# Kernel tuning notes

Hardware: AMD Instinct MI355X
Metric: run time of the kernel (lower is better)

The kernel has to match this reference:

```python
import math
import jax, jax.numpy as jnp
import numpy as np

B, L, C, H = 32, 320, 768, 12
LENS_T = 64
KEEP_RATIO = 0.7
AD_H = 64   # Mixer adapter bottleneck width (assumed bottleneck adapter)
EPS = 1e-5  # torch LayerNorm default


def _ln(x, g, b):
    m = jnp.mean(x, axis=-1, keepdims=True)
    v = jnp.mean((x - m) ** 2, axis=-1, keepdims=True)
    return (x - m) * jax.lax.rsqrt(v + EPS) * g + b


def _attention(x, qkv_w, proj_w, proj_b):
    b, l, c = x.shape
    dh = c // H
    qkv = (x @ qkv_w).reshape(b, l, 3, H, dh)
    q = jnp.transpose(qkv[:, :, 0], (0, 2, 1, 3))  # [B,H,L,Dh]
    k = jnp.transpose(qkv[:, :, 1], (0, 2, 1, 3))
    v = jnp.transpose(qkv[:, :, 2], (0, 2, 1, 3))
    a = jax.nn.softmax(jnp.einsum('bhid,bhjd->bhij', q * (dh ** -0.5), k), axis=-1)
    out = jnp.einsum('bhij,bhjd->bhid', a, v).transpose(0, 2, 1, 3).reshape(b, l, c)
    return out @ proj_w + proj_b, a


def _mixer(x, dw, db, uw, ub):
    return jax.nn.gelu(x @ dw + db, approximate=False) @ uw + ub


def _mlp(x, w1, b1, w2, b2):
    return jax.nn.gelu(x @ w1 + b1, approximate=False) @ w2 + b2


def _ce(attn, tokens, lens_t, lens_keep, gidx):
    # attn: [B,H,Lt+Ls,Lt+Ls]; average template->search block over heads and template rows
    attn_t = jnp.mean(attn[:, :, :lens_t, lens_t:], axis=(1, 2))  # [B, Ls]
    order = jnp.argsort(-attn_t, axis=1)                          # descending sort indices
    topk_idx, rest_idx = order[:, :lens_keep], order[:, lens_keep:]
    keep = jnp.take_along_axis(gidx, topk_idx, axis=1)
    removed = jnp.take_along_axis(gidx, rest_idx, axis=1)
    kept_tok = jnp.take_along_axis(tokens[:, lens_t:], topk_idx[..., None], axis=1)
    return jnp.concatenate([tokens[:, :lens_t], kept_tok], axis=1), keep, removed


def setup_inputs():
    key = jax.random.key(0)
    ks = jax.random.split(key, 12)
    p = lambda k, shape: jax.random.normal(k, shape, jnp.float32) * 0.02
    ls = L - LENS_T
    return {
        'x': jax.random.normal(ks[0], (B, L, C), jnp.float32),
        'xi': jax.random.normal(ks[1], (B, L, C), jnp.float32),
        'gi_t': jnp.arange(B * LENS_T, dtype=jnp.int32).reshape(B, LENS_T),
        'gi_ti': jnp.arange(B * LENS_T, dtype=jnp.int32).reshape(B, LENS_T),
        'gi_s': jnp.arange(B * ls, dtype=jnp.int32).reshape(B, ls),
        'gi_si': jnp.arange(B * ls, dtype=jnp.int32).reshape(B, ls),
        'layer': 0,
        'n1_g': jnp.ones((C,), jnp.float32), 'n1_b': jnp.zeros((C,), jnp.float32),
        'qkv_w': p(ks[2], (C, 3 * C)),
        'proj_w': p(ks[3], (C, C)), 'proj_b': jnp.zeros((C,), jnp.float32),
        'n2_g': jnp.ones((C,), jnp.float32), 'n2_b': jnp.zeros((C,), jnp.float32),
        'fc1_w': p(ks[4], (C, 4 * C)), 'fc1_b': jnp.zeros((4 * C,), jnp.float32),
        'fc2_w': p(ks[5], (4 * C, C)), 'fc2_b': jnp.zeros((C,), jnp.float32),
        'ad1_dw': p(ks[6], (C, AD_H)), 'ad1_db': jnp.zeros((AD_H,), jnp.float32),
        'ad1_uw': p(ks[7], (AD_H, C)), 'ad1_ub': jnp.zeros((C,), jnp.float32),
        'ad2_dw': p(ks[8], (C, AD_H)), 'ad2_db': jnp.zeros((AD_H,), jnp.float32),
        'ad2_uw': p(ks[9], (AD_H, C)), 'ad2_ub': jnp.zeros((C,), jnp.float32),
    }


def reference(x, xi, gi_t, gi_ti, gi_s, gi_si, layer,
              n1_g, n1_b, qkv_w, proj_w, proj_b, n2_g, n2_b,
              fc1_w, fc1_b, fc2_w, fc2_b,
              ad1_dw, ad1_db, ad1_uw, ad1_ub, ad2_dw, ad2_db, ad2_uw, ad2_ub):
    # layer not in {3,6,9}: Mixer-adapter path, then candidate elimination, then MLP
    xori = x
    xa, attn = _attention(_ln(x, n1_g, n1_b), qkv_w, proj_w, proj_b)
    x = x + xa + _mixer(_ln(xi, n1_g, n1_b), ad1_dw, ad1_db, ad1_uw, ad1_ub)
    xia, i_attn = _attention(_ln(xi, n1_g, n1_b), qkv_w, proj_w, proj_b)
    xi = xi + xia + _mixer(_ln(xori, n1_g, n1_b), ad1_dw, ad1_db, ad1_uw, ad1_ub)
    lens_t = gi_t.shape[1]
    lens_s = x.shape[1] - lens_t
    lens_keep = math.ceil(KEEP_RATIO * lens_s)  # 180
    x, gi_s, removed = _ce(attn, x, lens_t, lens_keep, gi_s)
    xi, gi_si, removedi = _ce(i_attn, xi, lens_t, lens_keep, gi_si)
    xori = x
    x = x + _mlp(_ln(x, n2_g, n2_b), fc1_w, fc1_b, fc2_w, fc2_b) \
          + _mixer(_ln(xi, n2_g, n2_b), ad2_dw, ad2_db, ad2_uw, ad2_ub)
    xi = xi + _mlp(_ln(xi, n2_g, n2_b), fc1_w, fc1_b, fc2_w, fc2_b) \
            + _mixer(_ln(xori, n2_g, n2_b), ad2_dw, ad2_db, ad2_uw, ad2_ub)
    return (x, gi_t, gi_s, removed, attn, xi, gi_ti, gi_si, removedi, i_attn)
```

## Files before the change

### kernel.cpp

```cpp
#include <hip/hip_runtime.h>
#include <hip/hip_bf16.h>

#define NB   32
#define LL   320
#define CC   768
#define NH   12
#define DHD  64
#define LT   64
#define LSN  256
#define NKEEP 180
#define NREM  76
#define LP   244
#define ADH  64
#define C4   3072

typedef __attribute__((ext_vector_type(8))) short s16x8;
typedef __attribute__((ext_vector_type(4))) float f32x4;

__device__ __forceinline__ ushort f2b(float f){
  union { __hip_bfloat16 h; ushort u; } cv;
  cv.h = __float2bfloat16(f);
  return cv.u;
}

__device__ __forceinline__ void glds16(const ushort* g, ushort* l){
  __builtin_amdgcn_global_load_lds(
      (const __attribute__((address_space(1))) void*)g,
      (__attribute__((address_space(3))) void*)l, 16, 0, 0);
}

__device__ __forceinline__ float blk_sum(float v, float* sh){
  #pragma unroll
  for (int o = 32; o > 0; o >>= 1) v += __shfl_down(v, o, 64);
  int w = threadIdx.x >> 6;
  if ((threadIdx.x & 63) == 0) sh[w] = v;
  __syncthreads();
  float r = sh[0] + sh[1] + sh[2] + sh[3];
  __syncthreads();
  return r;
}

__global__ __launch_bounds__(256) void ln_k(const float* __restrict__ x,
                                            const float* __restrict__ g,
                                            const float* __restrict__ be,
                                            float* __restrict__ y,
                                            ushort* __restrict__ yb,
                                            float* __restrict__ lnt){
  __shared__ float sh[4];
  size_t row = blockIdx.x;
  const float* xr = x + row * CC;
  int t = threadIdx.x;
  float v0 = xr[t], v1 = xr[t + 256], v2 = xr[t + 512];
  float m = blk_sum(v0 + v1 + v2, sh) * (1.0f / 768.0f);
  float d0 = v0 - m, d1 = v1 - m, d2 = v2 - m;
  float var = blk_sum(d0*d0 + d1*d1 + d2*d2, sh) * (1.0f / 768.0f);
  float rs = rsqrtf(var + 1e-5f);
  float o0 = d0 * rs * g[t]       + be[t];
  float o1 = d1 * rs * g[t + 256] + be[t + 256];
  float o2 = d2 * rs * g[t + 512] + be[t + 512];
  float* yr = y + row * CC;
  yr[t] = o0; yr[t + 256] = o1; yr[t + 512] = o2;
  if (yb){
    ushort* yr2 = yb + row * CC;
    yr2[t] = f2b(o0); yr2[t + 256] = f2b(o1); yr2[t + 512] = f2b(o2);
  }
  if (lnt){
    int i = (int)(row % LL);
    if (i < 64){
      float* lr = lnt + ((row / LL) * 64 + i) * CC;
      lr[t] = o0; lr[t + 256] = o1; lr[t + 512] = o2;
    }
  }
}

__global__ __launch_bounds__(256) void gemm2_k(
    const float* __restrict__ A1, const float* __restrict__ W1,
    float* __restrict__ C1, ushort* __restrict__ Cb1,
    const float* __restrict__ A2, const float* __restrict__ W2,
    float* __restrict__ C2,
    int K, int ldw, int ldc, int ysplit)
{
  __shared__ float As[32*128];
  __shared__ float Bs[32*128];
  const int t = threadIdx.x;
  const int tx = t & 15, ty = t >> 4;
  const int n0 = blockIdx.x * 128;
  const int yb = blockIdx.y;
  const float* A; const float* W; float* Cm; ushort* Cb; int m0;
  if (yb < ysplit){ A = A1; W = W1; Cm = C1; Cb = Cb1; m0 = yb * 128; }
  else            { A = A2; W = W2; Cm = C2; Cb = nullptr; m0 = (yb - ysplit) * 128; }

  float acc[8][8] = {};
  for (int k0 = 0; k0 < K; k0 += 32){
    #pragma unroll
    for (int q = 0; q < 4; q++){
      int idx = t + q*256;
      int m = idx & 127, kq = idx >> 7;
      float4 v = *reinterpret_cast<const float4*>(A + (size_t)(m0+m)*K + k0 + kq*4);
      As[(kq*4+0)*128 + m] = v.x; As[(kq*4+1)*128 + m] = v.y;
      As[(kq*4+2)*128 + m] = v.z; As[(kq*4+3)*128 + m] = v.w;
    }
    #pragma unroll
    for (int q = 0; q < 4; q++){
      int idx = t + q*256;
      int kr = idx >> 5, nq = idx & 31;
      float4 v = *reinterpret_cast<const float4*>(W + (size_t)(k0+kr)*ldw + n0 + nq*4);
      *reinterpret_cast<float4*>(&Bs[kr*128 + nq*4]) = v;
    }
    __syncthreads();
    #pragma unroll
    for (int kk = 0; kk < 32; kk++){
      float a[8], b[8];
      *reinterpret_cast<float4*>(&a[0]) = *reinterpret_cast<float4*>(&As[kk*128 + ty*4]);
      *reinterpret_cast<float4*>(&a[4]) = *reinterpret_cast<float4*>(&As[kk*128 + 64 + ty*4]);
      *reinterpret_cast<float4*>(&b[0]) = *reinterpret_cast<float4*>(&Bs[kk*128 + tx*4]);
      *reinterpret_cast<float4*>(&b[4]) = *reinterpret_cast<float4*>(&Bs[kk*128 + 64 + tx*4]);
      #pragma unroll
      for (int i = 0; i < 8; i++)
        #pragma unroll
        for (int j = 0; j < 8; j++)
          acc[i][j] = fmaf(a[i], b[j], acc[i][j]);
    }
    __syncthreads();
  }
  #pragma unroll
  for (int i = 0; i < 8; i++){
    int m = m0 + ty*4 + (i & 3) + (i >> 2) * 64;
    #pragma unroll
    for (int j = 0; j < 8; j++){
      int n = n0 + tx*4 + (j & 3) + (j >> 2) * 64;
      float v = acc[i][j];
      Cm[(size_t)m * ldc + n] = v;
      if (Cb) Cb[(size_t)m * ldc + n] = f2b(v);
    }
  }
}

template<bool GELU, bool ACC, bool OBF>
__global__ __launch_bounds__(256) void mg_k(
    const ushort* __restrict__ A, const ushort* __restrict__ Wt,
    const float* __restrict__ bias, void* __restrict__ Cp,
    int M, int N, int K,
    const float* __restrict__ res0, const float* __restrict__ res1, int Mhalf,
    const ushort* __restrict__ A2_0, const ushort* __restrict__ A2_1,
    const ushort* __restrict__ W2t, int K2, const float* __restrict__ bias2,
    void* __restrict__ Cp1)
{
  __shared__ __align__(16) ushort Asm[128*32];
  __shared__ __align__(16) ushort Bsm[128*32];
  const int t = threadIdx.x;
  const int m0 = blockIdx.y * 128, n0 = blockIdx.x * 128;
  const int wave = t >> 6, lane = t & 63;
  const int wrow = wave >> 1, wcol = wave & 1;
  const int lr = lane & 15, ks = lane >> 4;
  const int srow = lane >> 2, scp = lane & 3;

  f32x4 acc[4][4];
  #pragma unroll
  for (int i = 0; i < 4; i++)
    #pragma unroll
    for (int j = 0; j < 4; j++)
      #pragma unroll
      for (int r = 0; r < 4; r++) acc[i][j][r] = 0.f;

  const int nseg = W2t ? 2 : 1;
  for (int seg = 0; seg < nseg; seg++){
    const ushort* Abase; const ushort* Bbase; int ldA, ldB, Ks;
    if (seg == 0){
      Abase = A + (size_t)m0 * K; ldA = K; Bbase = Wt; ldB = K; Ks = K;
    } else {
      Abase = (res1 && m0 >= Mhalf) ? (A2_1 + (size_t)(m0 - Mhalf) * K2)
                                    : (A2_0 + (size_t)m0 * K2);
      ldA = K2; Bbase = W2t; ldB = K2; Ks = K2;
    }
    for (int k0 = 0; k0 < Ks; k0 += 32){
      #pragma unroll
      for (int q = 0; q < 2; q++){
        int r16 = wave*32 + q*16;
        int row = r16 + srow;
        int sch = scp ^ ((row >> 1) & 3);
        glds16(Abase + (size_t)row * ldA + k0 + sch*8, &Asm[r16*32]);
        int rbn = n0 + row; if (rbn > N-1) rbn = N-1;
        glds16(Bbase + (size_t)rbn * ldB + k0 + sch*8, &Bsm[r16*32]);
      }
      __syncthreads();
      s16x8 af[4], bf[4];
      #pragma unroll
      for (int f = 0; f < 4; f++){
        int ra = wrow*64 + f*16 + lr;
        af[f] = *reinterpret_cast<const s16x8*>(&Asm[ra*32 + ((ks ^ ((ra>>1)&3))<<3)]);
        int rbn = wcol*64 + f*16 + lr;
        bf[f] = *reinterpret_cast<const s16x8*>(&Bsm[rbn*32 + ((ks ^ ((rbn>>1)&3))<<3)]);
      }
      #pragma unroll
      for (int i = 0; i < 4; i++)
        #pragma unroll
        for (int j = 0; j < 4; j++)
          acc[i][j] = __builtin_amdgcn_mfma_f32_16x16x32_bf16(af[i], bf[j], acc[i][j], 0, 0, 0);
      __syncthreads();
    }
  }
  #pragma unroll
  for (int i = 0; i < 4; i++){
    int mb = m0 + wrow*64 + i*16 + ks*4;
    #pragma unroll
    for (int j = 0; j < 4; j++){
      int n = n0 + wcol*64 + j*16 + lr;
      if (n >= N) continue;
      float bv = (bias ? bias[n] : 0.0f) + (bias2 ? bias2[n] : 0.0f);
      #pragma unroll
      for (int r = 0; r < 4; r++){
        int mrow = mb + r;
        float v = acc[i][j][r] + bv;
        if (GELU) v = 0.5f * v * (1.0f + erff(v * 0.70710678118654752f));
        if (res0){
          if (res1 && mrow >= Mhalf) v += res1[(size_t)(mrow - Mhalf) * N + n];
          else                       v += res0[(size_t)mrow * N + n];
        }
        if (Cp1 && mrow >= Mhalf){
          size_t idx = (size_t)(mrow - Mhalf) * N + n;
          if (OBF)      ((ushort*)Cp1)[idx] = f2b(v);
          else if (ACC) ((float*)Cp1)[idx] += v;
          else          ((float*)Cp1)[idx]  = v;
        } else {
          size_t idx = (size_t)mrow * N + n;
          if (OBF)      ((ushort*)Cp)[idx] = f2b(v);
          else if (ACC) ((float*)Cp)[idx] += v;
          else          ((float*)Cp)[idx]  = v;
        }
      }
    }
  }
}

__global__ __launch_bounds__(256) void tconv_k(const float* __restrict__ W,
                                               ushort* __restrict__ Wt,
                                               int K, int N, int ldw, int colOff){
  __shared__ float tile[32][33];
  int t = threadIdx.x;
  int tx = t & 31, ty = t >> 5;
  int k0 = blockIdx.y * 32, n0 = blockIdx.x * 32;
  #pragma unroll
  for (int q = 0; q < 4; q++)
    tile[ty + 8*q][tx] = W[(size_t)(k0 + ty + 8*q) * ldw + colOff + n0 + tx];
  __syncthreads();
  #pragma unroll
  for (int q = 0; q < 4; q++)
    Wt[(size_t)(n0 + ty + 8*q) * K + k0 + tx] = f2b(tile[tx][ty + 8*q]);
}

__global__ __launch_bounds__(256) void scorest_k(const float* __restrict__ qt,
                                                 const float* __restrict__ kf,
                                                 float* __restrict__ p0,
                                                 float* __restrict__ p1){
  __shared__ float Qs[16][65];
  __shared__ float Ks[16][65];
  const int t = threadIdx.x, tx = t & 15, ty = t >> 4;
  const int s = blockIdx.y;
  const int bh = blockIdx.z; const int b = bh / NH, h = bh % NH;
  const int j0 = blockIdx.x * 64;
  float* sc = s ? p1 : p0;
  const float* qts = qt + (size_t)s * NB * 64 * CC;
  const float* kfs = kf + (size_t)s * NB * LL * CC;
  const size_t qbase = (size_t)b * 64 * CC + (size_t)h * 64;
  const size_t kbase = (size_t)b * LL * CC + (size_t)h * 64;
  const int lkk = t & 15, lmm = t >> 4;
  float acc[4][4] = {};
  for (int d0 = 0; d0 < DHD; d0 += 16){
    #pragma unroll
    for (int q = 0; q < 4; q++)
      Qs[lkk][lmm + 16*q] = qts[qbase + (size_t)(lmm + 16*q) * CC + d0 + lkk];
    #pragma unroll
    for (int q = 0; q < 4; q++)
      Ks[lkk][lmm + 16*q] = kfs[kbase + (size_t)(j0 + lmm + 16*q) * CC + d0 + lkk];
    __syncthreads();
    #pragma unroll
    for (int kk = 0; kk < 16; kk++){
      float a[4], b2[4];
      #pragma unroll
      for (int i = 0; i < 4; i++) a[i] = Qs[kk][ty*4 + i];
      #pragma unroll
      for (int j = 0; j < 4; j++) b2[j] = Ks[kk][tx*4 + j];
      #pragma unroll
      for (int i = 0; i < 4; i++)
        #pragma unroll
        for (int j = 0; j < 4; j++)
          acc[i][j] = fmaf(a[i], b2[j], acc[i][j]);
    }
    __syncthreads();
  }
  #pragma unroll
  for (int i = 0; i < 4; i++)
    #pragma unroll
    for (int j = 0; j < 4; j++)
      sc[((size_t)bh * LL + ty*4 + i) * LL + j0 + tx*4 + j] = acc[i][j] * 0.125f;
}

__global__ __launch_bounds__(256) void sqs_k(const ushort* __restrict__ qv,
                                             const ushort* __restrict__ kb,
                                             float* __restrict__ p0,
                                             float* __restrict__ p1){
  __shared__ ushort Qs[64][72];
  __shared__ ushort Ks[64][72];
  const int t = threadIdx.x;
  const int it = blockIdx.x, bh = blockIdx.y, s = blockIdx.z;
  const int b = bh / NH, h = bh % NH;
  const int w = t >> 6, lane = t & 63;
  const int lr = lane & 15, ks = lane >> 4;
  float* sc = s ? p1 : p0;
  const int qrow0 = s * NB * LL + b * LL + 64 + it * 64;
  const int krow0 = s * NB * LL + b * LL;

  #pragma unroll
  for (int q = 0; q < 4; q++){
    int idx = t + q*256;
    int row = idx >> 4, dv = idx & 15;
    *reinterpret_cast<ushort4*>(&Qs[row][dv*4]) =
      *reinterpret_cast<const ushort4*>(qv + (size_t)(qrow0 + row) * 1536 + h*64 + dv*4);
  }

  f32x4 acc[5][4];
  #pragma unroll
  for (int jt = 0; jt < 5; jt++)
    #pragma unroll
    for (int n = 0; n < 4; n++)
      #pragma unroll
      for (int r = 0; r < 4; r++) acc[jt][n][r] = 0.f;

  for (int jt = 0; jt < 5; jt++){
    __syncthreads();
    #pragma unroll
    for (int q = 0; q < 4; q++){
      int idx = t + q*256;
      int row = idx >> 4, dv = idx & 15;
      *reinterpret_cast<ushort4*>(&Ks[row][dv*4]) =
        *reinterpret_cast<const ushort4*>(kb + (size_t)(krow0 + jt*64 + row) * CC + h*64 + dv*4);
    }
    __syncthreads();
    #pragma unroll
    for (int n = 0; n < 4; n++)
      #pragma unroll
      for (int kt = 0; kt < 2; kt++){
        s16x8 a  = *reinterpret_cast<const s16x8*>(&Qs[w*16 + lr][kt*32 + ks*8]);
        s16x8 bb = *reinterpret_cast<const s16x8*>(&Ks[n*16 + lr][kt*32 + ks*8]);
        acc[jt][n] = __builtin_amdgcn_mfma_f32_16x16x32_bf16(a, bb, acc[jt][n], 0, 0, 0);
      }
  }
  #pragma unroll
  for (int jt = 0; jt < 5; jt++)
    #pragma unroll
    for (int n = 0; n < 4; n++)
      #pragma unroll
      for (int r = 0; r < 4; r++) acc[jt][n][r] *= 0.125f;
  #pragma unroll
  for (int r = 0; r < 4; r++){
    float mx = -3.4e38f;
    #pragma unroll
    for (int jt = 0; jt < 5; jt++)
      #pragma unroll
      for (int n = 0; n < 4; n++) mx = fmaxf(mx, acc[jt][n][r]);
    #pragma unroll
    for (int o = 1; o < 16; o <<= 1) mx = fmaxf(mx, __shfl_xor(mx, o, 64));
    float sum = 0.f;
    #pragma unroll
    for (int jt = 0; jt < 5; jt++)
      #pragma unroll
      for (int n = 0; n < 4; n++){
        float e = expf(acc[jt][n][r] - mx);
        acc[jt][n][r] = e; sum += e;
      }
    #pragma unroll
    for (int o = 1; o < 16; o <<= 1) sum += __shfl_xor(sum, o, 64);
    float inv = 1.0f / sum;
    size_t rowbase = ((size_t)bh * LL + 64 + it*64 + w*16 + ks*4 + r) * LL;
    #pragma unroll
    for (int jt = 0; jt < 5; jt++)
      #pragma unroll
      for (int n = 0; n < 4; n++)
        sc[rowbase + jt*64 + n*16 + lr] = acc[jt][n][r] * inv;
  }
}

__global__ __launch_bounds__(256) void softmaxt_k(float* __restrict__ p0,
                                                  float* __restrict__ p1){
  const int lane = threadIdx.x & 63;
  const int s = blockIdx.x / (NB*NH*16);
  const int bx = blockIdx.x % (NB*NH*16);
  const int bh = bx >> 4;
  const int i0 = (bx & 15) * 4;
  float* sc = s ? p1 : p0;
  const size_t row = (size_t)bh * LL + i0 + (threadIdx.x >> 6);
  float* sr = sc + row * LL;
  float v[5]; float mx = -3.4e38f;
  #pragma unroll
  for (int i = 0; i < 5; i++){ v[i] = sr[lane + 64*i]; mx = fmaxf(mx, v[i]); }
  #pragma unroll
  for (int o = 32; o > 0; o >>= 1) mx = fmaxf(mx, __shfl_xor(mx, o, 64));
  float s2 = 0.f;
  #pragma unroll
  for (int i = 0; i < 5; i++){ v[i] = expf(v[i] - mx); s2 += v[i]; }
  #pragma unroll
  for (int o = 32; o > 0; o >>= 1) s2 += __shfl_xor(s2, o, 64);
  float inv = 1.0f / s2;
  #pragma unroll
  for (int i = 0; i < 5; i++) sr[lane + 64*i] = v[i] * inv;
}

__global__ __launch_bounds__(256) void attnt1_k(const float* __restrict__ p0,
                                                const float* __restrict__ p1,
                                                double* __restrict__ pp){
  int g = blockIdx.x;
  int s = g / (NB*NH), bh = g % (NB*NH);
  int j = threadIdx.x;
  const float* probs = s ? p1 : p0;
  double sum = 0.0;
  for (int i = 0; i < LT; i++)
    sum += (double)probs[((size_t)bh * LL + i) * LL + 64 + j];
  pp[(size_t)g * LSN + j] = sum;
}
__global__ __launch_bounds__(256) void attnt2_k(const double* __restrict__ pp,
                                                float* __restrict__ at){
  int g = blockIdx.x;
  int j = threadIdx.x;
  double sum = 0.0;
  for (int h = 0; h < NH; h++)
    sum += pp[((size_t)g * NH + h) * LSN + j];
  at[g * LSN + j] = (float)(sum * (1.0 / 768.0));
}

__global__ __launch_bounds__(256) void pvm_k(const float* __restrict__ p0,
                                             const float* __restrict__ p1,
                                             const ushort* __restrict__ qv,
                                             ushort* __restrict__ pvb){
  __shared__ ushort Pa[64][72];
  __shared__ ushort Vt[64][72];
  const int t = threadIdx.x;
  const int bh = blockIdx.y, s = blockIdx.z;
  const int b = bh / NH, h = bh % NH;
  const int i0 = blockIdx.x * 64;
  const int w = t >> 6, lane = t & 63;
  const int lr = lane & 15, ks = lane >> 4;
  const float* Ap = (s ? p1 : p0) + (size_t)bh * LL * LL;
  const int vrow0 = s * NB * LL + b * LL;
  ushort* pvs = pvb + (size_t)s * NB * LL * CC;

  f32x4 acc[4];
  #pragma unroll
  for (int n = 0; n < 4; n++)
    #pragma unroll
    for (int r = 0; r < 4; r++) acc[n][r] = 0.f;

  for (int jt = 0; jt < 5; jt++){
    int j0 = jt * 64;
    #pragma unroll
    for (int q = 0; q < 4; q++){
      int idx = t + q*256;
      int i = idx >> 4, jv = idx & 15;
      float4 v = *reinterpret_cast<const float4*>(Ap + (size_t)(i0 + i) * LL + j0 + jv*4);
      ushort4 u; u.x = f2b(v.x); u.y = f2b(v.y); u.z = f2b(v.z); u.w = f2b(v.w);
      *reinterpret_cast<ushort4*>(&Pa[i][jv*4]) = u;
    }
    #pragma unroll
    for (int q = 0; q < 4; q++){
      int idx = t + q*256;
      int j = idx >> 4, dv = idx & 15;
      ushort4 u = *reinterpret_cast<const ushort4*>(
          qv + (size_t)(vrow0 + j0 + j) * 1536 + 768 + h*64 + dv*4);
      Vt[dv*4+0][j] = u.x; Vt[dv*4+1][j] = u.y;
      Vt[dv*4+2][j] = u.z; Vt[dv*4+3][j] = u.w;
    }
    __syncthreads();
    #pragma unroll
    for (int n = 0; n < 4; n++)
      #pragma unroll
      for (int kt = 0; kt < 2; kt++){
        s16x8 a = *reinterpret_cast<const s16x8*>(&Pa[w*16 + lr][kt*32 + ks*8]);
        s16x8 bb = *reinterpret_cast<const s16x8*>(&Vt[n*16 + lr][kt*32 + ks*8]);
        acc[n] = __builtin_amdgcn_mfma_f32_16x16x32_bf16(a, bb, acc[n], 0, 0, 0);
      }
    __syncthreads();
  }
  #pragma unroll
  for (int n = 0; n < 4; n++)
    #pragma unroll
    for (int r = 0; r < 4; r++){
      int i = w*16 + ks*4 + r;
      int d = n*16 + lr;
      pvs[(size_t)(b * LL + i0 + i) * 768 + h*64 + d] = f2b(acc[n][r]);
    }
}

__global__ __launch_bounds__(256) void init_ord_k(int* __restrict__ ordbuf, int n){
  int i = blockIdx.x * 256 + threadIdx.x;
  if (i < n) ordbuf[i] = i & 255;
}

__global__ __launch_bounds__(256) void ce_rank_k(const float* __restrict__ at,
                                                 int* __restrict__ ordbuf){
  __shared__ float a[256];
  int b = blockIdx.x, t = threadIdx.x;
  a[t] = at[b * LSN + t];
  __syncthreads();
  float mine = a[t];
  int rank = 0;
  for (int k = 0; k < 256; k++){
    float ak = a[k];
    rank += (ak > mine) || (ak == mine && k < t);
  }
  if (rank >= 0 && rank < 256) ordbuf[b * LSN + rank] = t;
}

__global__ __launch_bounds__(256) void ce_emit2_k(const int* __restrict__ ordbuf,
                                                  const int* __restrict__ g0,
                                                  const int* __restrict__ g1,
                                                  const int* __restrict__ t0,
                                                  const int* __restrict__ t1,
                                                  float* __restrict__ keep0,
                                                  float* __restrict__ keep1,
                                                  float* __restrict__ rem0,
                                                  float* __restrict__ rem1,
                                                  float* __restrict__ git0,
                                                  float* __restrict__ git1){
  int g = blockIdx.x, t = threadIdx.x;
  int s = g / NB, b = g % NB;
  const int* gidx = s ? g1 : g0;
  const int* gt   = s ? t1 : t0;
  float* out_keep = s ? keep1 : keep0;
  float* out_rem  = s ? rem1 : rem0;
  float* out_git  = s ? git1 : git0;
  int o = ordbuf[(size_t)g * LSN + t];
  o = min(max(o, 0), 255);
  int idx = gidx[b * LSN + o];
  if (t < NKEEP) out_keep[b * NKEEP + t] = (float)idx;
  else           out_rem[b * NREM + (t - NKEEP)] = (float)idx;
  if (t < LT)    out_git[b * LT + t] = (float)gt[b * LT + t];
}

__global__ __launch_bounds__(256) void gather_k(const float* __restrict__ xnew,
                                                const int* __restrict__ ordbuf,
                                                float* __restrict__ x2){
  int g = blockIdx.x;
  int s = g / (NB*LP), r0 = g % (NB*LP);
  int b = r0 / LP, r = r0 % LP;
  int o = (r < LT) ? 0 : ordbuf[(size_t)(s*NB + b) * LSN + (r - LT)];
  o = min(max(o, 0), 255);
  int src = (r < LT) ? r : (LT + o);
  const float* sp = xnew + (size_t)s * NB * LL * CC + ((size_t)b * LL + src) * CC;
  float* d = x2 + (size_t)s * NB * LP * CC + (size_t)r0 * CC;
  for (int i = threadIdx.x; i < CC; i += 256) d[i] = sp[i];
}

__global__ void sentinel_k(float* __restrict__ d, float val, int n){
  int i = blockIdx.x * 256 + threadIdx.x;
  if (i < n) d[i] = val;
}

extern "C" void kernel_launch(void* const* d_in, const int* in_sizes, int n_in,
                              void* d_out, int out_size, void* d_ws, size_t ws_size,
                              hipStream_t stream) {
  float* out = (float*)d_out;
  float* ws  = (float*)d_ws;

  static const int EXP[26] = {
    7864320, 7864320, 2048, 2048, 8192, 8192, 1,
    768, 768, 1769472, 589824, 768, 768, 768,
    2359296, 3072, 2359296, 768,
    49152, 64, 49152, 768, 49152, 64, 49152, 768 };

  const void* P[26];
  bool ok = false;
  if (n_in == 26){
    bool m = true; int bad = -1;
    for (int i = 0; i < 26; i++) if (in_sizes[i] != EXP[i]){ m = false; bad = i; break; }
    if (m){ for (int i = 0; i < 26; i++) P[i] = d_in[i]; ok = true; }
    else { sentinel_k<<<16, 256, 0, stream>>>(out, 20000.0f + 16.0f*bad, 4096); return; }
  } else if (n_in == 25){
    bool m = true; int bad = -1;
    for (int i = 0; i < 25; i++){
      int j = (i < 6) ? i : i + 1;
      if (in_sizes[i] != EXP[j]){ m = false; bad = i; break; }
    }
    if (m){
      for (int j = 0; j < 26; j++) P[j] = (j == 6) ? nullptr : d_in[(j < 6) ? j : j - 1];
      ok = true;
    } else { sentinel_k<<<16, 256, 0, stream>>>(out, 20000.0f + 16.0f*bad, 4096); return; }
  }
  if (!ok){ sentinel_k<<<16, 256, 0, stream>>>(out, 10000.0f + 8.0f*n_in, 4096); return; }
  if (out_size != 90656768){
    sentinel_k<<<16, 256, 0, stream>>>(out, 60000.0f + (float)(out_size / 1000000), 4096); return;
  }

  const float* x      = (const float*)P[0];
  const float* xi     = (const float*)P[1];
  const int*   gi_t   = (const int*)P[2];
  const int*   gi_ti  = (const int*)P[3];
  const int*   gi_s   = (const int*)P[4];
  const int*   gi_si  = (const int*)P[5];
  const float* n1_g   = (const float*)P[7];
  const float* n1_b   = (const float*)P[8];
  const float* qkv_w  = (const float*)P[9];
  const float* proj_w = (const float*)P[10];
  const float* proj_b = (const float*)P[11];
  const float* n2_g   = (const float*)P[12];
  const float* n2_b   = (const float*)P[13];
  const float* fc1_w  = (const float*)P[14];
  const float* fc1_b  = (const float*)P[15];
  const float* fc2_w  = (const float*)P[16];
  const float* fc2_b  = (const float*)P[17];
  const float* ad1_dw = (const float*)P[18];
  const float* ad1_db = (const float*)P[19];
  const float* ad1_uw = (const float*)P[20];
  const float* ad1_ub = (const float*)P[21];
  const float* ad2_dw = (const float*)P[22];
  const float* ad2_db = (const float*)P[23];
  const float* ad2_uw = (const float*)P[24];
  const float* ad2_ub = (const float*)P[25];

  const size_t o_x     = 0;
  const size_t o_git   = 5996544;
  const size_t o_gis   = 5998592;
  const size_t o_rem   = 6004352;
  const size_t o_attn  = 6006784;
  const size_t o_xi    = 45328384;
  const size_t o_giti  = 51324928;
  const size_t o_gisi  = 51326976;
  const size_t o_remi  = 51332736;
  const size_t o_iattn = 51335168;

  const size_t BLC      = (size_t)NB * LL * CC;
  const size_t BPC      = (size_t)NB * LP * CC;
  const size_t off_ln   = 0;
  const size_t off_l1b  = off_ln  + 2*BLC;
  const size_t off_k    = off_l1b + BLC;
  const size_t off_qv   = off_k   + 2*BLC;
  const size_t off_kb   = off_qv  + 2*BLC;
  const size_t off_lnt  = off_kb  + BLC;
  const size_t off_qt   = off_lnt + 3145728;
  const size_t off_xnew = off_qt  + 3145728;
  const size_t off_l2b  = off_xnew+ 2*BLC;
  const size_t off_mixh = off_l2b + BPC;
  const size_t off_att  = off_mixh+ 655360;
  const size_t off_attp = off_att + 16384;
  const size_t off_ord  = off_attp+ 393216;
  const size_t off_wts  = off_ord + 16384;
  const size_t total_f  = off_wts + 3342336;
  if (ws_size < total_f * sizeof(float)){
    sentinel_k<<<16, 256, 0, stream>>>(out, 40000.0f + (float)(ws_size >> 20), 4096);
    return;
  }

  int* ordbuf = (int*)(ws + off_ord);
  double* attp = (double*)(ws + off_attp);
  ushort* wts = (ushort*)(ws + off_wts);
  ushort* Wt_q    = wts;
  ushort* Wt_v    = wts + 589824;
  ushort* Wt_proj = wts + 1179648;
  ushort* Wt_fc1  = wts + 1769472;
  ushort* Wt_fc2  = wts + 4128768;
  ushort* Wt_a1d  = wts + 6488064;
  ushort* Wt_a1u  = wts + 6537216;
  ushort* Wt_a2d  = wts + 6586368;
  ushort* Wt_a2u  = wts + 6635520;
  ushort* ln1b = (ushort*)(ws + off_l1b);
  ushort* qvb  = (ushort*)(ws + off_qv);
  ushort* kb   = (ushort*)(ws + off_kb);
  ushort* pvb  = (ushort*)(ws + off_k);
  ushort* ln2b = (ushort*)(ws + off_l2b);
  ushort* mixhb= (ushort*)(ws + off_mixh);

  float* p0 = out + o_attn;
  float* p1 = out + o_iattn;

  tconv_k<<<dim3(24, 24), 256, 0, stream>>>(qkv_w,  Wt_q,    768, 768,  2304, 0);
  tconv_k<<<dim3(24, 24), 256, 0, stream>>>(qkv_w,  Wt_v,    768, 768,  2304, 1536);
  tconv_k<<<dim3(24, 24), 256, 0, stream>>>(proj_w, Wt_proj, 768, 768,  768,  0);
  tconv_k<<<dim3(96, 24), 256, 0, stream>>>(fc1_w,  Wt_fc1,  768, 3072, 3072, 0);
  tconv_k<<<dim3(24, 96), 256, 0, stream>>>(fc2_w,  Wt_fc2,  3072, 768, 768,  0);
  tconv_k<<<dim3(2,  24), 256, 0, stream>>>(ad1_dw, Wt_a1d,  768, 64,   64,   0);
  tconv_k<<<dim3(24, 2 ), 256, 0, stream>>>(ad1_uw, Wt_a1u,  64,  768,  768,  0);
  tconv_k<<<dim3(2,  24), 256, 0, stream>>>(ad2_dw, Wt_a2d,  768, 64,   64,   0);
  tconv_k<<<dim3(24, 2 ), 256, 0, stream>>>(ad2_uw, Wt_a2u,  64,  768,  768,  0);

  ln_k<<<NB*LL, 256, 0, stream>>>(x,  n1_g, n1_b, ws + off_ln, ln1b, ws + off_lnt);
  ln_k<<<NB*LL, 256, 0, stream>>>(xi, n1_g, n1_b, ws + off_ln + BLC,
                                  ln1b + (size_t)NB*LL*CC,
                                  ws + off_lnt + (size_t)NB*64*CC);
  mg_k<true,false,true><<<dim3(1, 160), 256, 0, stream>>>(
      ln1b, Wt_a1d, ad1_db, mixhb, 2*NB*LL, ADH, CC,
      nullptr, nullptr, 0, nullptr, nullptr, nullptr, 0, nullptr, nullptr);
  gemm2_k<<<dim3(6, 192), 256, 0, stream>>>(
      ws + off_ln, qkv_w + 768, ws + off_k, kb,
      ws + off_lnt, qkv_w, ws + off_qt,
      CC, 2304, CC, 160);
  mg_k<false,false,true><<<dim3(12, 160), 256, 0, stream>>>(
      ln1b, Wt_q, nullptr, qvb, 2*NB*LL, 1536, CC,
      nullptr, nullptr, 0, nullptr, nullptr, nullptr, 0, nullptr, nullptr);

  scorest_k<<<dim3(5, 2, NB*NH), 256, 0, stream>>>(ws + off_qt, ws + off_k, p0, p1);
  sqs_k<<<dim3(4, NB*NH, 2), 256, 0, stream>>>(qvb, kb, p0, p1);
  softmaxt_k<<<2*NB*NH*16, 256, 0, stream>>>(p0, p1);
  attnt1_k<<<2*NB*NH, 256, 0, stream>>>(p0, p1, attp);
  attnt2_k<<<2*NB, 256, 0, stream>>>(attp, ws + off_att);

  pvm_k<<<dim3(5, NB*NH, 2), 256, 0, stream>>>(p0, p1, qvb, pvb);
  mg_k<false,false,false><<<dim3(6, 160), 256, 0, stream>>>(
      pvb, Wt_proj, proj_b, ws + off_xnew, 2*NB*LL, CC, CC,
      x, xi, NB*LL,
      mixhb + (size_t)NB*LL*ADH, mixhb, Wt_a1u, ADH, ad1_ub, nullptr);

  init_ord_k<<<(2*NB*LSN + 255)/256, 256, 0, stream>>>(ordbuf, 2*NB*LSN);
  ce_rank_k<<<2*NB, 256, 0, stream>>>(ws + off_att, ordbuf);
  ce_emit2_k<<<2*NB, 256, 0, stream>>>(
      ordbuf, gi_s, gi_si, gi_t, gi_ti,
      out + o_gis, out + o_gisi, out + o_rem, out + o_remi,
      out + o_git, out + o_giti);
  gather_k<<<2*NB*LP, 256, 0, stream>>>(ws + off_xnew, ordbuf, ws + off_ln);

  float* x2  = ws + off_ln;
  float* ln2 = ws + off_xnew;
  ushort* hidb   = (ushort*)(ws + off_k);
  ushort* mixh2b = mixhb;

  ln_k<<<2*NB*LP, 256, 0, stream>>>(x2, n2_g, n2_b, ln2, ln2b, nullptr);
  mg_k<true,false,true><<<dim3(1, 122), 256, 0, stream>>>(
      ln2b, Wt_a2d, ad2_db, mixh2b, 2*NB*LP, ADH, CC,
      nullptr, nullptr, 0, nullptr, nullptr, nullptr, 0, nullptr, nullptr);
  mg_k<true,false,true><<<dim3(24, 122), 256, 0, stream>>>(
      ln2b, Wt_fc1, fc1_b, hidb, 2*NB*LP, C4, CC,
      nullptr, nullptr, 0, nullptr, nullptr, nullptr, 0, nullptr, nullptr);

  mg_k<false,false,false><<<dim3(6, 122), 256, 0, stream>>>(
      hidb, Wt_fc2, fc2_b, out + o_x, 2*NB*LP, CC, C4,
      x2, x2 + BPC, NB*LP,
      mixh2b + (size_t)NB*LP*ADH, mixh2b, Wt_a2u, ADH, ad2_ub,
      out + o_xi);
}
```

Measured before the change: 1.348 ms.

## Merge independent launches into multi-job kernels and fold head-sum into softmax

Independent kernels are combined into single launches that pick their job from the block index. The nine weight transposes become one launch, the two first LayerNorms one, the K/Qt fp32 GEMM plus QV and adapter-down GEMMs one, the two score kernels one, and fc1 plus adapter-down one. The template-row partial sums move into the softmax kernel, so attnt1 goes away and the final reduction reads more partials (the workspace grows to hold them). ce_rank now builds the full order in shared memory, removing the init kernel. This cuts launch count and tail idle time, at the cost of heterogeneous blocks sharing one register and LDS budget.

```diff
diff --git a/kernel.cpp b/kernel.cpp
--- a/kernel.cpp
+++ b/kernel.cpp
@@ -40,15 +40,18 @@
   return r;
 }
 
-__global__ __launch_bounds__(256) void ln_k(const float* __restrict__ x,
-                                            const float* __restrict__ g,
-                                            const float* __restrict__ be,
-                                            float* __restrict__ y,
-                                            ushort* __restrict__ yb,
-                                            float* __restrict__ lnt){
+__global__ __launch_bounds__(256) void ln12_k(const float* __restrict__ x0,
+                                              const float* __restrict__ x1,
+                                              int rowsplit,
+                                              const float* __restrict__ g,
+                                              const float* __restrict__ be,
+                                              float* __restrict__ y,
+                                              ushort* __restrict__ yb,
+                                              float* __restrict__ lnt){
   __shared__ float sh[4];
-  size_t row = blockIdx.x;
-  const float* xr = x + row * CC;
+  int row = blockIdx.x;
+  const float* xr = (row < rowsplit) ? x0 + (size_t)row * CC
+                                     : x1 + (size_t)(row - rowsplit) * CC;
   int t = threadIdx.x;
   float v0 = xr[t], v1 = xr[t + 256], v2 = xr[t + 512];
   float m = blk_sum(v0 + v1 + v2, sh) * (1.0f / 768.0f);
@@ -58,37 +61,35 @@
   float o0 = d0 * rs * g[t]       + be[t];
   float o1 = d1 * rs * g[t + 256] + be[t + 256];
   float o2 = d2 * rs * g[t + 512] + be[t + 512];
-  float* yr = y + row * CC;
+  float* yr = y + (size_t)row * CC;
   yr[t] = o0; yr[t + 256] = o1; yr[t + 512] = o2;
   if (yb){
-    ushort* yr2 = yb + row * CC;
+    ushort* yr2 = yb + (size_t)row * CC;
     yr2[t] = f2b(o0); yr2[t + 256] = f2b(o1); yr2[t + 512] = f2b(o2);
   }
   if (lnt){
-    int i = (int)(row % LL);
+    int i = row % LL;
     if (i < 64){
-      float* lr = lnt + ((row / LL) * 64 + i) * CC;
+      float* lr = lnt + ((size_t)(row / LL) * 64 + i) * CC;
       lr[t] = o0; lr[t + 256] = o1; lr[t + 512] = o2;
     }
   }
 }
 
-__global__ __launch_bounds__(256) void gemm2_k(
+__device__ __forceinline__ void f32gemm_body(
+    float* As, float* Bs, int bx, int by,
     const float* __restrict__ A1, const float* __restrict__ W1,
     float* __restrict__ C1, ushort* __restrict__ Cb1,
     const float* __restrict__ A2, const float* __restrict__ W2,
     float* __restrict__ C2,
     int K, int ldw, int ldc, int ysplit)
 {
-  __shared__ float As[32*128];
-  __shared__ float Bs[32*128];
   const int t = threadIdx.x;
   const int tx = t & 15, ty = t >> 4;
-  const int n0 = blockIdx.x * 128;
-  const int yb = blockIdx.y;
+  const int n0 = bx * 128;
   const float* A; const float* W; float* Cm; ushort* Cb; int m0;
-  if (yb < ysplit){ A = A1; W = W1; Cm = C1; Cb = Cb1; m0 = yb * 128; }
-  else            { A = A2; W = W2; Cm = C2; Cb = nullptr; m0 = (yb - ysplit) * 128; }
+  if (by < ysplit){ A = A1; W = W1; Cm = C1; Cb = Cb1; m0 = by * 128; }
+  else            { A = A2; W = W2; Cm = C2; Cb = nullptr; m0 = (by - ysplit) * 128; }
 
   float acc[8][8] = {};
   for (int k0 = 0; k0 < K; k0 += 32){
@@ -137,7 +138,8 @@
 }
 
 template<bool GELU, bool ACC, bool OBF>
-__global__ __launch_bounds__(256) void mg_k(
+__device__ __forceinline__ void mg_body(
+    ushort* Asm, ushort* Bsm, int bx, int by,
     const ushort* __restrict__ A, const ushort* __restrict__ Wt,
     const float* __restrict__ bias, void* __restrict__ Cp,
     int M, int N, int K,
@@ -146,10 +148,8 @@
     const ushort* __restrict__ W2t, int K2, const float* __restrict__ bias2,
     void* __restrict__ Cp1)
 {
-  __shared__ __align__(16) ushort Asm[128*32];
-  __shared__ __align__(16) ushort Bsm[128*32];
   const int t = threadIdx.x;
-  const int m0 = blockIdx.y * 128, n0 = blockIdx.x * 128;
+  const int m0 = by * 128, n0 = bx * 128;
   const int wave = t >> 6, lane = t & 63;
   const int wrow = wave >> 1, wcol = wave & 1;
   const int lr = lane & 15, ks = lane >> 4;
@@ -233,33 +233,81 @@
   }
 }
 
-__global__ __launch_bounds__(256) void tconv_k(const float* __restrict__ W,
-                                               ushort* __restrict__ Wt,
-                                               int K, int N, int ldw, int colOff){
-  __shared__ float tile[32][33];
-  int t = threadIdx.x;
-  int tx = t & 31, ty = t >> 5;
-  int k0 = blockIdx.y * 32, n0 = blockIdx.x * 32;
-  #pragma unroll
-  for (int q = 0; q < 4; q++)
-    tile[ty + 8*q][tx] = W[(size_t)(k0 + ty + 8*q) * ldw + colOff + n0 + tx];
-  __syncthreads();
-  #pragma unroll
-  for (int q = 0; q < 4; q++)
-    Wt[(size_t)(n0 + ty + 8*q) * K + k0 + tx] = f2b(tile[tx][ty + 8*q]);
-}
-
-__global__ __launch_bounds__(256) void scorest_k(const float* __restrict__ qt,
-                                                 const float* __restrict__ kf,
-                                                 float* __restrict__ p0,
-                                                 float* __restrict__ p1){
-  __shared__ float Qs[16][65];
-  __shared__ float Ks[16][65];
+template<bool GELU, bool ACC, bool OBF>
+__global__ __launch_bounds__(256) void mg_k(
+    const ushort* __restrict__ A, const ushort* __restrict__ Wt,
+    const float* __restrict__ bias, void* __restrict__ Cp,
+    int M, int N, int K,
+    const float* __restrict__ res0, const float* __restrict__ res1, int Mhalf,
+    const ushort* __restrict__ A2_0, const ushort* __restrict__ A2_1,
+    const ushort* __restrict__ W2t, int K2, const float* __restrict__ bias2,
+    void* __restrict__ Cp1)
+{
+  __shared__ __align__(16) ushort shm[8192];
+  mg_body<GELU,ACC,OBF>(shm, shm + 4096, blockIdx.x, blockIdx.y,
+                        A, Wt, bias, Cp, M, N, K, res0, res1, Mhalf,
+                        A2_0, A2_1, W2t, K2, bias2, Cp1);
+}
+
+#define FA_F32 1152
+#define FA_QV  1920
+__global__ __launch_bounds__(256) void fuseA_k(
+    const float* __restrict__ lnf, const float* __restrict__ qkvw,
+    float* __restrict__ kf, ushort* __restrict__ kbm,
+    const float* __restrict__ lnt, float* __restrict__ qt,
+    const ushort* __restrict__ ln1b, const ushort* __restrict__ Wt_q,
+    ushort* __restrict__ qvb,
+    const ushort* __restrict__ Wt_a1d, const float* __restrict__ a1db,
+    ushort* __restrict__ mixhb)
+{
+  __shared__ __align__(16) float sh[8192];
+  int bid = blockIdx.x;
+  if (bid < FA_F32){
+    f32gemm_body(sh, sh + 4096, bid % 6, bid / 6,
+                 lnf, qkvw + 768, kf, kbm, lnt, qkvw, qt,
+                 CC, 2304, CC, 160);
+  } else if (bid < FA_F32 + FA_QV){
+    int b2 = bid - FA_F32;
+    mg_body<false,false,true>((ushort*)sh, (ushort*)sh + 4096, b2 % 12, b2 / 12,
+        ln1b, Wt_q, nullptr, qvb, 2*NB*LL, 1536, CC,
+        nullptr, nullptr, 0, nullptr, nullptr, nullptr, 0, nullptr, nullptr);
+  } else {
+    int by = bid - FA_F32 - FA_QV;
+    mg_body<true,false,true>((ushort*)sh, (ushort*)sh + 4096, 0, by,
+        ln1b, Wt_a1d, a1db, mixhb, 2*NB*LL, ADH, CC,
+        nullptr, nullptr, 0, nullptr, nullptr, nullptr, 0, nullptr, nullptr);
+  }
+}
+
+__global__ __launch_bounds__(256) void fuseB_k(
+    const ushort* __restrict__ ln2b, const ushort* __restrict__ Wt_fc1,
+    const float* __restrict__ fc1b, ushort* __restrict__ hidb,
+    const ushort* __restrict__ Wt_a2d, const float* __restrict__ a2db,
+    ushort* __restrict__ mixh2b)
+{
+  __shared__ __align__(16) ushort shm[8192];
+  int bid = blockIdx.x;
+  if (bid < 24*122){
+    mg_body<true,false,true>(shm, shm + 4096, bid % 24, bid / 24,
+        ln2b, Wt_fc1, fc1b, hidb, 2*NB*LP, C4, CC,
+        nullptr, nullptr, 0, nullptr, nullptr, nullptr, 0, nullptr, nullptr);
+  } else {
+    mg_body<true,false,true>(shm, shm + 4096, 0, bid - 24*122,
+        ln2b, Wt_a2d, a2db, mixh2b, 2*NB*LP, ADH, CC,
+        nullptr, nullptr, 0, nullptr, nullptr, nullptr, 0, nullptr, nullptr);
+  }
+}
+
+__device__ __forceinline__ void scorest_body(
+    float* shf, int jt, int s, int bh,
+    const float* __restrict__ qt, const float* __restrict__ kf,
+    float* __restrict__ sc)
+{
+  float* Qs = shf;
+  float* Ks = shf + 16*65;
   const int t = threadIdx.x, tx = t & 15, ty = t >> 4;
-  const int s = blockIdx.y;
-  const int bh = blockIdx.z; const int b = bh / NH, h = bh % NH;
-  const int j0 = blockIdx.x * 64;
-  float* sc = s ? p1 : p0;
+  const int b = bh / NH, h = bh % NH;
+  const int j0 = jt * 64;
   const float* qts = qt + (size_t)s * NB * 64 * CC;
   const float* kfs = kf + (size_t)s * NB * LL * CC;
   const size_t qbase = (size_t)b * 64 * CC + (size_t)h * 64;
@@ -269,18 +317,18 @@
   for (int d0 = 0; d0 < DHD; d0 += 16){
     #pragma unroll
     for (int q = 0; q < 4; q++)
-      Qs[lkk][lmm + 16*q] = qts[qbase + (size_t)(lmm + 16*q) * CC + d0 + lkk];
+      Qs[lkk*65 + lmm + 16*q] = qts[qbase + (size_t)(lmm + 16*q) * CC + d0 + lkk];
     #pragma unroll
     for (int q = 0; q < 4; q++)
-      Ks[lkk][lmm + 16*q] = kfs[kbase + (size_t)(j0 + lmm + 16*q) * CC + d0 + lkk];
+      Ks[lkk*65 + lmm + 16*q] = kfs[kbase + (size_t)(j0 + lmm + 16*q) * CC + d0 + lkk];
     __syncthreads();
     #pragma unroll
     for (int kk = 0; kk < 16; kk++){
       float a[4], b2[4];
       #pragma unroll
-      for (int i = 0; i < 4; i++) a[i] = Qs[kk][ty*4 + i];
-      #pragma unroll
-      for (int j = 0; j < 4; j++) b2[j] = Ks[kk][tx*4 + j];
+      for (int i = 0; i < 4; i++) a[i] = Qs[kk*65 + ty*4 + i];
+      #pragma unroll
+      for (int j = 0; j < 4; j++) b2[j] = Ks[kk*65 + tx*4 + j];
       #pragma unroll
       for (int i = 0; i < 4; i++)
         #pragma unroll
@@ -296,18 +344,15 @@
       sc[((size_t)bh * LL + ty*4 + i) * LL + j0 + tx*4 + j] = acc[i][j] * 0.125f;
 }
 
-__global__ __launch_bounds__(256) void sqs_k(const ushort* __restrict__ qv,
-                                             const ushort* __restrict__ kb,
-                                             float* __restrict__ p0,
-                                             float* __restrict__ p1){
-  __shared__ ushort Qs[64][72];
-  __shared__ ushort Ks[64][72];
+__device__ __forceinline__ void sqs_body(
+    ushort* Qs, ushort* Ks, int it, int bh, int s,
+    const ushort* __restrict__ qv, const ushort* __restrict__ kb,
+    float* __restrict__ sc)
+{
   const int t = threadIdx.x;
-  const int it = blockIdx.x, bh = blockIdx.y, s = blockIdx.z;
   const int b = bh / NH, h = bh % NH;
   const int w = t >> 6, lane = t & 63;
   const int lr = lane & 15, ks = lane >> 4;
-  float* sc = s ? p1 : p0;
   const int qrow0 = s * NB * LL + b * LL + 64 + it * 64;
   const int krow0 = s * NB * LL + b * LL;
 
@@ -315,7 +360,7 @@
   for (int q = 0; q < 4; q++){
     int idx = t + q*256;
     int row = idx >> 4, dv = idx & 15;
-    *reinterpret_cast<ushort4*>(&Qs[row][dv*4]) =
+    *reinterpret_cast<ushort4*>(&Qs[row*72 + dv*4]) =
       *reinterpret_cast<const ushort4*>(qv + (size_t)(qrow0 + row) * 1536 + h*64 + dv*4);
   }
 
@@ -333,7 +378,7 @@
     for (int q = 0; q < 4; q++){
       int idx = t + q*256;
       int row = idx >> 4, dv = idx & 15;
-      *reinterpret_cast<ushort4*>(&Ks[row][dv*4]) =
+      *reinterpret_cast<ushort4*>(&Ks[row*72 + dv*4]) =
         *reinterpret_cast<const ushort4*>(kb + (size_t)(krow0 + jt*64 + row) * CC + h*64 + dv*4);
     }
     __syncthreads();
@@ -341,8 +386,8 @@
     for (int n = 0; n < 4; n++)
       #pragma unroll
       for (int kt = 0; kt < 2; kt++){
-        s16x8 a  = *reinterpret_cast<const s16x8*>(&Qs[w*16 + lr][kt*32 + ks*8]);
-        s16x8 bb = *reinterpret_cast<const s16x8*>(&Ks[n*16 + lr][kt*32 + ks*8]);
+        s16x8 a  = *reinterpret_cast<const s16x8*>(&Qs[(w*16 + lr)*72 + kt*32 + ks*8]);
+        s16x8 bb = *reinterpret_cast<const s16x8*>(&Ks[(n*16 + lr)*72 + kt*32 + ks*8]);
         acc[jt][n] = __builtin_amdgcn_mfma_f32_16x16x32_bf16(a, bb, acc[jt][n], 0, 0, 0);
       }
   }
@@ -381,15 +426,36 @@
   }
 }
 
+#define SC_T 3840
+__global__ __launch_bounds__(256) void scoresf_k(
+    const float* __restrict__ qt, const float* __restrict__ kf,
+    const ushort* __restrict__ qv, const ushort* __restrict__ kb,
+    float* __restrict__ p0, float* __restrict__ p1)
+{
+  __shared__ __align__(16) ushort shm[2*64*72];
+  int bid = blockIdx.x;
+  if (bid < SC_T){
+    int jt = bid % 5; int r = bid / 5; int s = r & 1; int bh = r >> 1;
+    scorest_body((float*)shm, jt, s, bh, qt, kf, s ? p1 : p0);
+  } else {
+    int b2 = bid - SC_T;
+    int it = b2 & 3; int r = b2 >> 2; int bh = r % (NB*NH); int s = r / (NB*NH);
+    sqs_body(shm, shm + 64*72, it, bh, s, qv, kb, s ? p1 : p0);
+  }
+}
+
 __global__ __launch_bounds__(256) void softmaxt_k(float* __restrict__ p0,
-                                                  float* __restrict__ p1){
+                                                  float* __restrict__ p1,
+                                                  double* __restrict__ pp){
+  __shared__ float a4[4][256];
   const int lane = threadIdx.x & 63;
+  const int w = threadIdx.x >> 6;
   const int s = blockIdx.x / (NB*NH*16);
   const int bx = blockIdx.x % (NB*NH*16);
   const int bh = bx >> 4;
   const int i0 = (bx & 15) * 4;
   float* sc = s ? p1 : p0;
-  const size_t row = (size_t)bh * LL + i0 + (threadIdx.x >> 6);
+  const size_t row = (size_t)bh * LL + i0 + w;
   float* sr = sc + row * LL;
   float v[5]; float mx = -3.4e38f;
   #pragma unroll
@@ -403,28 +469,30 @@
   for (int o = 32; o > 0; o >>= 1) s2 += __shfl_xor(s2, o, 64);
   float inv = 1.0f / s2;
   #pragma unroll
-  for (int i = 0; i < 5; i++) sr[lane + 64*i] = v[i] * inv;
-}
-
-__global__ __launch_bounds__(256) void attnt1_k(const float* __restrict__ p0,
-                                                const float* __restrict__ p1,
-                                                double* __restrict__ pp){
-  int g = blockIdx.x;
-  int s = g / (NB*NH), bh = g % (NB*NH);
-  int j = threadIdx.x;
-  const float* probs = s ? p1 : p0;
-  double sum = 0.0;
-  for (int i = 0; i < LT; i++)
-    sum += (double)probs[((size_t)bh * LL + i) * LL + 64 + j];
-  pp[(size_t)g * LSN + j] = sum;
-}
+  for (int i = 0; i < 5; i++){
+    float p = v[i] * inv;
+    sr[lane + 64*i] = p;
+    if (i >= 1) a4[w][lane + 64*(i-1)] = p;
+  }
+  __syncthreads();
+  int t = threadIdx.x;
+  double ssum = ((double)a4[0][t] + (double)a4[1][t])
+              + ((double)a4[2][t] + (double)a4[3][t]);
+  double s0 = (double)a4[0][t];
+  s0 += (double)a4[1][t]; s0 += (double)a4[2][t]; s0 += (double)a4[3][t];
+  (void)ssum;
+  pp[(size_t)blockIdx.x * 256 + t] = s0;
+}
+
 __global__ __launch_bounds__(256) void attnt2_k(const double* __restrict__ pp,
                                                 float* __restrict__ at){
   int g = blockIdx.x;
+  int s = g / NB, b = g % NB;
   int j = threadIdx.x;
   double sum = 0.0;
   for (int h = 0; h < NH; h++)
-    sum += pp[((size_t)g * NH + h) * LSN + j];
+    for (int p = 0; p < 16; p++)
+      sum += pp[((size_t)(s*NB*NH + b*NH + h) * 16 + p) * 256 + j];
   at[g * LSN + j] = (float)(sum * (1.0 / 768.0));
 }
 
@@ -490,16 +558,13 @@
     }
 }
 
-__global__ __launch_bounds__(256) void init_ord_k(int* __restrict__ ordbuf, int n){
-  int i = blockIdx.x * 256 + threadIdx.x;
-  if (i < n) ordbuf[i] = i & 255;
-}
-
 __global__ __launch_bounds__(256) void ce_rank_k(const float* __restrict__ at,
                                                  int* __restrict__ ordbuf){
   __shared__ float a[256];
+  __shared__ int ord[256];
   int b = blockIdx.x, t = threadIdx.x;
   a[t] = at[b * LSN + t];
+  ord[t] = t;
   __syncthreads();
   float mine = a[t];
   int rank = 0;
@@ -507,7 +572,9 @@
     float ak = a[k];
     rank += (ak > mine) || (ak == mine && k < t);
   }
-  if (rank >= 0 && rank < 256) ordbuf[b * LSN + rank] = t;
+  if (rank >= 0 && rank < 256) ord[rank] = t;
+  __syncthreads();
+  ordbuf[(size_t)b * LSN + t] = ord[t];
 }
 
 __global__ __launch_bounds__(256) void ce_emit2_k(const int* __restrict__ ordbuf,
@@ -548,6 +615,29 @@
   const float* sp = xnew + (size_t)s * NB * LL * CC + ((size_t)b * LL + src) * CC;
   float* d = x2 + (size_t)s * NB * LP * CC + (size_t)r0 * CC;
   for (int i = threadIdx.x; i < CC; i += 256) d[i] = sp[i];
+}
+
+struct TJ { const float* W; ushort* Wt; int K, N, ldw, colOff, blk0; };
+struct TJobs { TJ j[9]; };
+__global__ __launch_bounds__(256) void tconvm_k(TJobs jobs){
+  __shared__ float tile[32][33];
+  int bid = blockIdx.x;
+  int ji = 0;
+  #pragma unroll
+  for (int i = 1; i < 9; i++) if (bid >= jobs.j[i].blk0) ji = i;
+  TJ jb = jobs.j[ji];
+  int local = bid - jb.blk0;
+  int txl = jb.N / 32;
+  int n0 = (local % txl) * 32, k0 = (local / txl) * 32;
+  int t = threadIdx.x;
+  int tx = t & 31, ty = t >> 5;
+  #pragma unroll
+  for (int q = 0; q < 4; q++)
+    tile[ty + 8*q][tx] = jb.W[(size_t)(k0 + ty + 8*q) * jb.ldw + jb.colOff + n0 + tx];
+  __syncthreads();
+  #pragma unroll
+  for (int q = 0; q < 4; q++)
+    jb.Wt[(size_t)(n0 + ty + 8*q) * jb.K + k0 + tx] = f2b(tile[tx][ty + 8*q]);
 }
 
 __global__ void sentinel_k(float* __restrict__ d, float val, int n){
@@ -641,7 +731,7 @@
   const size_t off_mixh = off_l2b + BPC;
   const size_t off_att  = off_mixh+ 655360;
   const size_t off_attp = off_att + 16384;
-  const size_t off_ord  = off_attp+ 393216;
+  const size_t off_ord  = off_attp+ 6291456;
   const size_t off_wts  = off_ord + 16384;
   const size_t total_f  = off_wts + 3342336;
   if (ws_size < total_f * sizeof(float)){
@@ -671,35 +761,28 @@
   float* p0 = out + o_attn;
   float* p1 = out + o_iattn;
 
-  tconv_k<<<dim3(24, 24), 256, 0, stream>>>(qkv_w,  Wt_q,    768, 768,  2304, 0);
-  tconv_k<<<dim3(24, 24), 256, 0, stream>>>(qkv_w,  Wt_v,    768, 768,  2304, 1536);
-  tconv_k<<<dim3(24, 24), 256, 0, stream>>>(proj_w, Wt_proj, 768, 768,  768,  0);
-  tconv_k<<<dim3(96, 24), 256, 0, stream>>>(fc1_w,  Wt_fc1,  768, 3072, 3072, 0);
-  tconv_k<<<dim3(24, 96), 256, 0, stream>>>(fc2_w,  Wt_fc2,  3072, 768, 768,  0);
-  tconv_k<<<dim3(2,  24), 256, 0, stream>>>(ad1_dw, Wt_a1d,  768, 64,   64,   0);
-  tconv_k<<<dim3(24, 2 ), 256, 0, stream>>>(ad1_uw, Wt_a1u,  64,  768,  768,  0);
-  tconv_k<<<dim3(2,  24), 256, 0, stream>>>(ad2_dw, Wt_a2d,  768, 64,   64,   0);
-  tconv_k<<<dim3(24, 2 ), 256, 0, stream>>>(ad2_uw, Wt_a2u,  64,  768,  768,  0);
-
-  ln_k<<<NB*LL, 256, 0, stream>>>(x,  n1_g, n1_b, ws + off_ln, ln1b, ws + off_lnt);
-  ln_k<<<NB*LL, 256, 0, stream>>>(xi, n1_g, n1_b, ws + off_ln + BLC,
-                                  ln1b + (size_t)NB*LL*CC,
-                                  ws + off_lnt + (size_t)NB*64*CC);
-  mg_k<true,false,true><<<dim3(1, 160), 256, 0, stream>>>(
-      ln1b, Wt_a1d, ad1_db, mixhb, 2*NB*LL, ADH, CC,
-      nullptr, nullptr, 0, nullptr, nullptr, nullptr, 0, nullptr, nullptr);
-  gemm2_k<<<dim3(6, 192), 256, 0, stream>>>(
-      ws + off_ln, qkv_w + 768, ws + off_k, kb,
-      ws + off_lnt, qkv_w, ws + off_qt,
-      CC, 2304, CC, 160);
-  mg_k<false,false,true><<<dim3(12, 160), 256, 0, stream>>>(
-      ln1b, Wt_q, nullptr, qvb, 2*NB*LL, 1536, CC,
-      nullptr, nullptr, 0, nullptr, nullptr, nullptr, 0, nullptr, nullptr);
-
-  scorest_k<<<dim3(5, 2, NB*NH), 256, 0, stream>>>(ws + off_qt, ws + off_k, p0, p1);
-  sqs_k<<<dim3(4, NB*NH, 2), 256, 0, stream>>>(qvb, kb, p0, p1);
-  softmaxt_k<<<2*NB*NH*16, 256, 0, stream>>>(p0, p1);
-  attnt1_k<<<2*NB*NH, 256, 0, stream>>>(p0, p1, attp);
+  TJobs tj;
+  tj.j[0] = { qkv_w,  Wt_q,    768, 768,  2304, 0,    0 };
+  tj.j[1] = { qkv_w,  Wt_v,    768, 768,  2304, 1536, 576 };
+  tj.j[2] = { proj_w, Wt_proj, 768, 768,  768,  0,    1152 };
+  tj.j[3] = { fc1_w,  Wt_fc1,  768, 3072, 3072, 0,    1728 };
+  tj.j[4] = { fc2_w,  Wt_fc2,  3072, 768, 768,  0,    4032 };
+  tj.j[5] = { ad1_dw, Wt_a1d,  768, 64,   64,   0,    6336 };
+  tj.j[6] = { ad1_uw, Wt_a1u,  64,  768,  768,  0,    6384 };
+  tj.j[7] = { ad2_dw, Wt_a2d,  768, 64,   64,   0,    6432 };
+  tj.j[8] = { ad2_uw, Wt_a2u,  64,  768,  768,  0,    6480 };
+  tconvm_k<<<6528, 256, 0, stream>>>(tj);
+
+  ln12_k<<<2*NB*LL, 256, 0, stream>>>(x, xi, NB*LL, n1_g, n1_b,
+                                      ws + off_ln, ln1b, ws + off_lnt);
+
+  fuseA_k<<<FA_F32 + FA_QV + 160, 256, 0, stream>>>(
+      ws + off_ln, qkv_w, ws + off_k, kb, ws + off_lnt, ws + off_qt,
+      ln1b, Wt_q, qvb, Wt_a1d, ad1_db, mixhb);
+
+  scoresf_k<<<SC_T + 3072, 256, 0, stream>>>(ws + off_qt, ws + off_k, qvb, kb, p0, p1);
+
+  softmaxt_k<<<2*NB*NH*16, 256, 0, stream>>>(p0, p1, attp);
   attnt2_k<<<2*NB, 256, 0, stream>>>(attp, ws + off_att);
 
   pvm_k<<<dim3(5, NB*NH, 2), 256, 0, stream>>>(p0, p1, qvb, pvb);
@@ -708,7 +791,6 @@
       x, xi, NB*LL,
       mixhb + (size_t)NB*LL*ADH, mixhb, Wt_a1u, ADH, ad1_ub, nullptr);
 
-  init_ord_k<<<(2*NB*LSN + 255)/256, 256, 0, stream>>>(ordbuf, 2*NB*LSN);
   ce_rank_k<<<2*NB, 256, 0, stream>>>(ws + off_att, ordbuf);
   ce_emit2_k<<<2*NB, 256, 0, stream>>>(
       ordbuf, gi_s, gi_si, gi_t, gi_ti,
@@ -721,14 +803,9 @@
   ushort* hidb   = (ushort*)(ws + off_k);
   ushort* mixh2b = mixhb;
 
-  ln_k<<<2*NB*LP, 256, 0, stream>>>(x2, n2_g, n2_b, ln2, ln2b, nullptr);
-  mg_k<true,false,true><<<dim3(1, 122), 256, 0, stream>>>(
-      ln2b, Wt_a2d, ad2_db, mixh2b, 2*NB*LP, ADH, CC,
-      nullptr, nullptr, 0, nullptr, nullptr, nullptr, 0, nullptr, nullptr);
-  mg_k<true,false,true><<<dim3(24, 122), 256, 0, stream>>>(
-      ln2b, Wt_fc1, fc1_b, hidb, 2*NB*LP, C4, CC,
-      nullptr, nullptr, 0, nullptr, nullptr, nullptr, 0, nullptr, nullptr);
-
+  ln12_k<<<2*NB*LP, 256, 0, stream>>>(x2, x2, 2*NB*LP, n2_g, n2_b, ln2, ln2b, nullptr);
+  fuseB_k<<<24*122 + 122, 256, 0, stream>>>(
+      ln2b, Wt_fc1, fc1_b, hidb, Wt_a2d, ad2_db, mixh2b);
   mg_k<false,false,false><<<dim3(6, 122), 256, 0, stream>>>(
       hidb, Wt_fc2, fc2_b, out + o_x, 2*NB*LP, CC, C4,
       x2, x2 + BPC, NB*LP,
```

Result: no change. 1.367 ms (+1.4%).
